# Performance work log

Measured on AMD Instinct MI355X. Metric: run time of the kernel, lower is better.

Reference implementation:

```python
import jax, jax.numpy as jnp
import numpy as np

N_NODES = 50000


def _add_self_loops(edge_index, num_nodes):
    loop = jnp.arange(num_nodes, dtype=edge_index.dtype)
    src = jnp.concatenate([edge_index[0], loop])
    dst = jnp.concatenate([edge_index[1], loop])
    return src, dst


def _gcn_norm(src, dst, num_nodes, dtype):
    # symmetric normalization: deg^{-1/2}[src] * deg^{-1/2}[dst]
    deg = jax.ops.segment_sum(jnp.ones_like(dst, dtype=dtype), dst,
                              num_segments=num_nodes)
    dinv = jnp.where(deg > 0, jax.lax.rsqrt(deg), 0.0).astype(dtype)
    return dinv[src] * dinv[dst]


def _gcn_conv(x, src, dst, norm, W, b, num_nodes):
    h = x @ W                                  # [N, out]
    msg = norm[:, None] * h[src]               # [E', out] gather
    agg = jax.ops.segment_sum(msg, dst, num_segments=num_nodes)  # scatter-add
    return agg + b


def setup_inputs() -> dict:
    key = jax.random.key(0)
    k1, k2, k3, k4 = jax.random.split(key, 4)
    x = jax.random.normal(k1, (N_NODES, 64), dtype=jnp.float32)
    edge_index = jax.random.randint(k2, (2, 800000), 0, N_NODES, dtype=jnp.int64)
    W1 = jax.random.normal(k3, (64, 64), dtype=jnp.float32) * (1.0 / np.sqrt(64))
    b1 = jnp.zeros((64,), dtype=jnp.float32)
    W2 = jax.random.normal(k4, (64, 37), dtype=jnp.float32) * (1.0 / np.sqrt(64))
    b2 = jnp.zeros((37,), dtype=jnp.float32)
    return {"x": x, "edge_index": edge_index, "W1": W1, "b1": b1,
            "W2": W2, "b2": b2}


def reference(x, edge_index, W1, b1, W2, b2):
    n = x.shape[0]
    src, dst = _add_self_loops(edge_index, n)
    norm = _gcn_norm(src, dst, n, x.dtype)
    h = _gcn_conv(x, src, dst, norm, W1, b1, n)
    h = jax.nn.relu(h)
    out = _gcn_conv(h, src, dst, norm, W2, b2, n)
    return out
```

## Files before the change

### kernel.cpp

```cpp
#include <hip/hip_runtime.h>
#include <hip/hip_fp16.h>

#define F_OUT 37
#define BSHIFT 7
#define BSIZE 128
#define CAP 3072
#define STAGE_CAP 3072
#define XS_STRIDE 68

__device__ __forceinline__ short4 pack4(float a, float b, float c, float d) {
    union { __half2 h2[2]; short4 s; } u;
    u.h2[0] = __floats2half2_rn(a, b);
    u.h2[1] = __floats2half2_rn(c, d);
    return u.s;
}
__device__ __forceinline__ float4 unpack4(short4 v) {
    union { short4 s; __half2 h2[2]; } u;
    u.s = v;
    float2 lo = __half22float2(u.h2[0]);
    float2 hi = __half22float2(u.h2[1]);
    return make_float4(lo.x, lo.y, hi.x, hi.y);
}


__global__ void init_gcur(int* __restrict__ gcur, int nb) {
    int t = blockIdx.x * blockDim.x + threadIdx.x;
    if (t < nb) gcur[t * 16] = t * CAP;
}

__global__ __launch_bounds__(256) void bucketA(const int* __restrict__ src,
                                               const int* __restrict__ dst,
                                               int E, int C, int nb,
                                               int* __restrict__ gcur,
                                               unsigned* __restrict__ bedge) {
    __shared__ unsigned stage[STAGE_CAP];
    __shared__ int lcnt[400];
    __shared__ int lbase[400];
    int t = threadIdx.x;
    int e0 = blockIdx.x * C;
    int cnt = E - e0; if (cnt > C) cnt = C; if (cnt <= 0) return;

    for (int i = t; i < nb; i += 256) lcnt[i] = 0;
    __syncthreads();
    for (int i = t; i < cnt; i += 256) {
        int s = src[e0 + i], d = dst[e0 + i];
        int b = d >> BSHIFT;
        atomicAdd(&lcnt[b], 1);
        stage[i] = ((unsigned)b << 23) | ((unsigned)(d & (BSIZE - 1)) << 16) | (unsigned)s;
    }
    __syncthreads();
    for (int i = t; i < nb; i += 256)
        lbase[i] = lcnt[i] ? atomicAdd(&gcur[i * 16], lcnt[i]) : 0;
    __syncthreads();
    for (int i = t; i < nb; i += 256) lcnt[i] = 0;
    __syncthreads();
    for (int i = t; i < cnt; i += 256) {
        unsigned w = stage[i];
        int b = w >> 23;
        int pos = lbase[b] + atomicAdd(&lcnt[b], 1);
        bedge[pos] = w & 0x7FFFFFu;
    }
}

__global__ __launch_bounds__(512) void scan_buckets(const int* __restrict__ gcur,
                                                    int nb, int E, int n,
                                                    int* __restrict__ bstart,
                                                    int* __restrict__ rowptr) {
    __shared__ int s[512];
    int t = threadIdx.x;
    int v = (t < nb) ? (gcur[t * 16] - t * CAP) : 0;
    s[t] = v;
    __syncthreads();
    for (int o = 1; o < 512; o <<= 1) {
        int a = (t >= o) ? s[t - o] : 0;
        __syncthreads();
        s[t] += a;
        __syncthreads();
    }
    if (t < nb) bstart[t] = s[t] - v;
    if (t == 0) rowptr[n] = E;
}

__global__ __launch_bounds__(256) void bucketB(const unsigned* __restrict__ bedge,
                                               const int* __restrict__ gcur,
                                               const int* __restrict__ bstart,
                                               int n,
                                               int* __restrict__ rowptr,
                                               int* __restrict__ srcIdx,
                                               float* __restrict__ dinv) {
    __shared__ int hcnt[BSIZE], hoff[BSIZE], hcur[BSIZE], tmp[BSIZE];
    int b = blockIdx.x;
    int t = threadIdx.x;
    int cntb = gcur[b * 16] - b * CAP;
    int base = bstart[b];
    const unsigned* ed = bedge + (size_t)b * CAP;

    if (t < BSIZE) { hcnt[t] = 0; hcur[t] = 0; }
    __syncthreads();
    for (int i = t; i < cntb; i += 256) atomicAdd(&hcnt[ed[i] >> 16], 1);
    __syncthreads();
    if (t < BSIZE) tmp[t] = hcnt[t];
    __syncthreads();
    for (int o = 1; o < BSIZE; o <<= 1) {
        int a = (t < BSIZE && t >= o) ? tmp[t - o] : 0;
        __syncthreads();
        if (t < BSIZE) tmp[t] += a;
        __syncthreads();
    }
    if (t < BSIZE) hoff[t] = tmp[t] - hcnt[t];
    __syncthreads();
    int node = b * BSIZE + t;
    if (t < BSIZE && node < n) {
        rowptr[node] = base + hoff[t];
        dinv[node] = rsqrtf(1.0f + (float)hcnt[t]);
    }
    for (int i = t; i < cntb; i += 256) {
        unsigned w = ed[i];
        int dloc = w >> 16;
        int pos = base + hoff[dloc] + atomicAdd(&hcur[dloc], 1);
        srcIdx[pos] = (int)(w & 0xFFFFu);
    }
}


#define MICRO_STEP(XI, ACC)                                                    \
    do {                                                                       \
        ACC[0] += XI.x * w0.x; ACC[1] += XI.x * w0.y;                          \
        ACC[2] += XI.x * w0.z; ACC[3] += XI.x * w0.w;                          \
        ACC[0] += XI.y * w1.x; ACC[1] += XI.y * w1.y;                          \
        ACC[2] += XI.y * w1.z; ACC[3] += XI.y * w1.w;                          \
        ACC[0] += XI.z * w2.x; ACC[1] += XI.z * w2.y;                          \
        ACC[2] += XI.z * w2.z; ACC[3] += XI.z * w2.w;                          \
        ACC[0] += XI.w * w3.x; ACC[1] += XI.w * w3.y;                          \
        ACC[2] += XI.w * w3.z; ACC[3] += XI.w * w3.w;                          \
    } while (0)

__global__ __launch_bounds__(256, 4) void gemm64(const float* __restrict__ x,
                                                 const float* __restrict__ W,
                                                 const float* __restrict__ dinv,
                                                 short4* __restrict__ hsv, int n) {
    __shared__ float Xs[64 * XS_STRIDE];
    __shared__ float Ws[64 * 64];
    int t = threadIdx.x;
    const float4* W4 = (const float4*)W;
#pragma unroll
    for (int i = 0; i < 4; ++i)
        ((float4*)Ws)[t + i * 256] = W4[t + i * 256];
    int row0 = blockIdx.x * 64;
#pragma unroll
    for (int i = 0; i < 4; ++i) {
        int idx = i * 256 + t;
        int r = idx >> 4, k4 = idx & 15;
        int grow = row0 + r;
        float4 v = (grow < n) ? ((const float4*)x)[(size_t)grow * 16 + k4]
                              : make_float4(0.f, 0.f, 0.f, 0.f);
        *(float4*)&Xs[r * XS_STRIDE + k4 * 4] = v;
    }
    __syncthreads();

    int tc = t & 15, tr = t >> 4;
    float a0[4] = {0.f, 0.f, 0.f, 0.f};
    float a1[4] = {0.f, 0.f, 0.f, 0.f};
    float a2[4] = {0.f, 0.f, 0.f, 0.f};
    float a3[4] = {0.f, 0.f, 0.f, 0.f};

#pragma unroll 2
    for (int k = 0; k < 64; k += 4) {
        float4 w0 = *(const float4*)&Ws[(k + 0) * 64 + 4 * tc];
        float4 w1 = *(const float4*)&Ws[(k + 1) * 64 + 4 * tc];
        float4 w2 = *(const float4*)&Ws[(k + 2) * 64 + 4 * tc];
        float4 w3 = *(const float4*)&Ws[(k + 3) * 64 + 4 * tc];
        float4 x0 = *(const float4*)&Xs[(4 * tr + 0) * XS_STRIDE + k];
        float4 x1 = *(const float4*)&Xs[(4 * tr + 1) * XS_STRIDE + k];
        float4 x2 = *(const float4*)&Xs[(4 * tr + 2) * XS_STRIDE + k];
        float4 x3 = *(const float4*)&Xs[(4 * tr + 3) * XS_STRIDE + k];
        MICRO_STEP(x0, a0);
        MICRO_STEP(x1, a1);
        MICRO_STEP(x2, a2);
        MICRO_STEP(x3, a3);
    }

#define STORE64(ACC, R)                                                        \
    do {                                                                       \
        int row = row0 + 4 * tr + (R);                                         \
        if (row < n) {                                                         \
            float dd = dinv[row];                                              \
            hsv[(size_t)row * 16 + tc] =                                       \
                pack4(ACC[0] * dd, ACC[1] * dd, ACC[2] * dd, ACC[3] * dd);     \
        }                                                                      \
    } while (0)
    STORE64(a0, 0); STORE64(a1, 1); STORE64(a2, 2); STORE64(a3, 3);
#undef STORE64
}

__global__ __launch_bounds__(256, 4) void gemm37(const short4* __restrict__ h1v,
                                                 const float* __restrict__ W,
                                                 short4* __restrict__ g40v, int n) {
    __shared__ float Xs[64 * XS_STRIDE];
    __shared__ float Ws[64 * 64];
    int t = threadIdx.x;
    for (int i = t; i < 64 * 64; i += 256) {
        int k = i >> 6, c = i & 63;
        Ws[i] = (c < F_OUT) ? W[k * F_OUT + c] : 0.f;
    }
    int row0 = blockIdx.x * 64;
#pragma unroll
    for (int i = 0; i < 4; ++i) {
        int idx = i * 256 + t;
        int r = idx >> 4, k4 = idx & 15;
        int grow = row0 + r;
        float4 v = (grow < n) ? unpack4(h1v[(size_t)grow * 16 + k4])
                              : make_float4(0.f, 0.f, 0.f, 0.f);
        *(float4*)&Xs[r * XS_STRIDE + k4 * 4] = v;
    }
    __syncthreads();

    int tc = t & 15, tr = t >> 4;
    float a0[4] = {0.f, 0.f, 0.f, 0.f};
    float a1[4] = {0.f, 0.f, 0.f, 0.f};
    float a2[4] = {0.f, 0.f, 0.f, 0.f};
    float a3[4] = {0.f, 0.f, 0.f, 0.f};

#pragma unroll 2
    for (int k = 0; k < 64; k += 4) {
        float4 w0 = *(const float4*)&Ws[(k + 0) * 64 + 4 * tc];
        float4 w1 = *(const float4*)&Ws[(k + 1) * 64 + 4 * tc];
        float4 w2 = *(const float4*)&Ws[(k + 2) * 64 + 4 * tc];
        float4 w3 = *(const float4*)&Ws[(k + 3) * 64 + 4 * tc];
        float4 x0 = *(const float4*)&Xs[(4 * tr + 0) * XS_STRIDE + k];
        float4 x1 = *(const float4*)&Xs[(4 * tr + 1) * XS_STRIDE + k];
        float4 x2 = *(const float4*)&Xs[(4 * tr + 2) * XS_STRIDE + k];
        float4 x3 = *(const float4*)&Xs[(4 * tr + 3) * XS_STRIDE + k];
        MICRO_STEP(x0, a0);
        MICRO_STEP(x1, a1);
        MICRO_STEP(x2, a2);
        MICRO_STEP(x3, a3);
    }

    if (tc < 10) {
        int row = row0 + 4 * tr;
        if (row < n)
            g40v[(size_t)row * 10 + tc] = pack4(a0[0], a0[1], a0[2], a0[3]);
        if (row + 1 < n)
            g40v[(size_t)(row + 1) * 10 + tc] = pack4(a1[0], a1[1], a1[2], a1[3]);
        if (row + 2 < n)
            g40v[(size_t)(row + 2) * 10 + tc] = pack4(a2[0], a2[1], a2[2], a2[3]);
        if (row + 3 < n)
            g40v[(size_t)(row + 3) * 10 + tc] = pack4(a3[0], a3[1], a3[2], a3[3]);
    }
}


#define ACCP4(A, B, C, D)                                                      \
    acc.x += (A.x + B.x) + (C.x + D.x);                                        \
    acc.y += (A.y + B.y) + (C.y + D.y);                                        \
    acc.z += (A.z + B.z) + (C.z + D.z);                                        \
    acc.w += (A.w + B.w) + (C.w + D.w);

__global__ void agg64_kernel(const int* __restrict__ rowptr,
                             const int* __restrict__ srcIdx,
                             const float* __restrict__ dinv,
                             const short4* __restrict__ hsv,
                             const float* __restrict__ bias,
                             short4* __restrict__ outv, int n) {
    int t = blockIdx.x * blockDim.x + threadIdx.x;
    int d = t >> 4, sub = t & 15;
    if (d >= n) return;
    int gbase = threadIdx.x & 48;
    float4 acc = unpack4(hsv[(size_t)d * 16 + sub]);
    int beg = rowptr[d], end = rowptr[d + 1];
    int j = beg;
#define LD64(Q) float4 v##Q = unpack4(hsv[(size_t)__shfl(myIdx, gbase + Q) * 16 + sub]);
    for (; j + 16 <= end; j += 16) {
        int myIdx = srcIdx[j + sub];
        LD64(0) LD64(1) LD64(2) LD64(3) LD64(4) LD64(5) LD64(6) LD64(7)
        LD64(8) LD64(9) LD64(10) LD64(11) LD64(12) LD64(13) LD64(14) LD64(15)
        ACCP4(v0, v1, v2, v3) ACCP4(v4, v5, v6, v7)
        ACCP4(v8, v9, v10, v11) ACCP4(v12, v13, v14, v15)
    }
    if (j + 8 <= end) {
        int myIdx = srcIdx[j + sub];
        LD64(0) LD64(1) LD64(2) LD64(3) LD64(4) LD64(5) LD64(6) LD64(7)
        ACCP4(v0, v1, v2, v3) ACCP4(v4, v5, v6, v7)
        j += 8;
    }
    if (j + 4 <= end) {
        int s0 = srcIdx[j], s1 = srcIdx[j + 1], s2 = srcIdx[j + 2], s3 = srcIdx[j + 3];
        float4 v0 = unpack4(hsv[(size_t)s0 * 16 + sub]);
        float4 v1 = unpack4(hsv[(size_t)s1 * 16 + sub]);
        float4 v2 = unpack4(hsv[(size_t)s2 * 16 + sub]);
        float4 v3 = unpack4(hsv[(size_t)s3 * 16 + sub]);
        ACCP4(v0, v1, v2, v3)
        j += 4;
    }
    for (; j < end; ++j) {
        float4 v = unpack4(hsv[(size_t)srcIdx[j] * 16 + sub]);
        acc.x += v.x; acc.y += v.y; acc.z += v.z; acc.w += v.w;
    }
#undef LD64
    float dd = dinv[d];
    float4 b = ((const float4*)bias)[sub];
    outv[(size_t)d * 16 + sub] =
        pack4(fmaxf(acc.x * dd + b.x, 0.f) * dd,
              fmaxf(acc.y * dd + b.y, 0.f) * dd,
              fmaxf(acc.z * dd + b.z, 0.f) * dd,
              fmaxf(acc.w * dd + b.w, 0.f) * dd);
}

__global__ void agg40_kernel(const int* __restrict__ rowptr,
                             const int* __restrict__ srcIdx,
                             const float* __restrict__ dinv,
                             const short4* __restrict__ g4v,
                             const float* __restrict__ bias,
                             float* __restrict__ out, int n) {
    int t = blockIdx.x * blockDim.x + threadIdx.x;
    int d = t >> 4, sub = t & 15;
    if (d >= n) return;
    int gbase = threadIdx.x & 48;
    bool act = sub < 10;
    float4 acc = make_float4(0.f, 0.f, 0.f, 0.f);
    if (act) acc = unpack4(g4v[(size_t)d * 10 + sub]);
    int beg = rowptr[d], end = rowptr[d + 1];
    int j = beg;
#define SH40(Q) int s##Q = __shfl(myIdx, gbase + Q);
#define G40(Q)  float4 v##Q = unpack4(g4v[(size_t)s##Q * 10 + sub]);
    for (; j + 16 <= end; j += 16) {
        int myIdx = srcIdx[j + sub];
        SH40(0) SH40(1) SH40(2) SH40(3) SH40(4) SH40(5) SH40(6) SH40(7)
        SH40(8) SH40(9) SH40(10) SH40(11) SH40(12) SH40(13) SH40(14) SH40(15)
        if (act) {
            G40(0) G40(1) G40(2) G40(3) G40(4) G40(5) G40(6) G40(7)
            G40(8) G40(9) G40(10) G40(11) G40(12) G40(13) G40(14) G40(15)
            ACCP4(v0, v1, v2, v3) ACCP4(v4, v5, v6, v7)
            ACCP4(v8, v9, v10, v11) ACCP4(v12, v13, v14, v15)
        }
    }
    if (j + 8 <= end) {
        int myIdx = srcIdx[j + sub];
        SH40(0) SH40(1) SH40(2) SH40(3) SH40(4) SH40(5) SH40(6) SH40(7)
        if (act) {
            G40(0) G40(1) G40(2) G40(3) G40(4) G40(5) G40(6) G40(7)
            ACCP4(v0, v1, v2, v3) ACCP4(v4, v5, v6, v7)
        }
        j += 8;
    }
    if (j + 4 <= end) {
        int s0 = srcIdx[j], s1 = srcIdx[j + 1], s2 = srcIdx[j + 2], s3 = srcIdx[j + 3];
        if (act) {
            float4 v0 = unpack4(g4v[(size_t)s0 * 10 + sub]);
            float4 v1 = unpack4(g4v[(size_t)s1 * 10 + sub]);
            float4 v2 = unpack4(g4v[(size_t)s2 * 10 + sub]);
            float4 v3 = unpack4(g4v[(size_t)s3 * 10 + sub]);
            ACCP4(v0, v1, v2, v3)
        }
        j += 4;
    }
    for (; j < end; ++j) {
        int s = srcIdx[j];
        if (act) {
            float4 v = unpack4(g4v[(size_t)s * 10 + sub]);
            acc.x += v.x; acc.y += v.y; acc.z += v.z; acc.w += v.w;
        }
    }
#undef SH40
#undef G40
    if (act) {
        float dd = dinv[d];
        int c0 = 4 * sub;
        float* o = &out[(size_t)d * F_OUT + c0];
        o[0] = acc.x * dd + bias[c0];
        if (c0 + 1 < F_OUT) o[1] = acc.y * dd + bias[c0 + 1];
        if (c0 + 2 < F_OUT) o[2] = acc.z * dd + bias[c0 + 2];
        if (c0 + 3 < F_OUT) o[3] = acc.w * dd + bias[c0 + 3];
    }
}

extern "C" void kernel_launch(void* const* d_in, const int* in_sizes, int n_in,
                              void* d_out, int out_size, void* d_ws, size_t ws_size,
                              hipStream_t stream) {
    const float* x  = (const float*)d_in[0];
    const int*   ei = (const int*)d_in[1];
    const float* W1 = (const float*)d_in[2];
    const float* b1 = (const float*)d_in[3];
    const float* W2 = (const float*)d_in[4];
    const float* b2 = (const float*)d_in[5];
    float* out = (float*)d_out;

    const int n = in_sizes[0] / 64;
    const int E = in_sizes[1] / 2;
    const int* src = ei;
    const int* dst = ei + E;

    const int nb = (n + BSIZE - 1) >> BSHIFT;
    const int nblkA = (E + STAGE_CAP - 1) / STAGE_CAP;
    const int C = (E + nblkA - 1) / nblkA;

    char* p = (char*)d_ws;
    int*   gcur   = (int*)p;   p += (size_t)nb * 16 * 4;
    int*   bstart = (int*)p;   p += (size_t)((nb + 3) & ~3) * 4;
    int*   rowptr = (int*)p;   p += (size_t)(n + 4) * 4;
    float* dinv   = (float*)p; p += (size_t)n * 4;
    int*   srcIdx = (int*)p;   p += (size_t)(E + 16) * 4;
    short4* hsv   = (short4*)p; p += (size_t)n * 64 * 2;
    short4* h1v   = (short4*)p; p += (size_t)n * 64 * 2;
    unsigned* bedge = (unsigned*)hsv;
    short4* g40v  = hsv;

    init_gcur<<<(nb + 255) / 256, 256, 0, stream>>>(gcur, nb);
    bucketA<<<nblkA, 256, 0, stream>>>(src, dst, E, C, nb, gcur, bedge);
    scan_buckets<<<1, 512, 0, stream>>>(gcur, nb, E, n, bstart, rowptr);
    bucketB<<<nb, 256, 0, stream>>>(bedge, gcur, bstart, n, rowptr, srcIdx, dinv);

    const int gemmBlocks = (n + 63) / 64;
    const int aggBlocks  = (n * 16 + 255) / 256;

    gemm64<<<gemmBlocks, 256, 0, stream>>>(x, W1, dinv, hsv, n);
    agg64_kernel<<<aggBlocks, 256, 0, stream>>>(rowptr, srcIdx, dinv, hsv, b1, h1v, n);

    gemm37<<<gemmBlocks, 256, 0, stream>>>(h1v, W2, g40v, n);
    agg40_kernel<<<aggBlocks, 256, 0, stream>>>(rowptr, srcIdx, dinv, g40v, b2, out, n);
}
```

Measured before the change: 114.9 us.

## Split layer-1 feature table into two column slices for cache-friendly aggregation

Splits the 64-wide half-precision hidden features into two 32-column tables, each 3.2MB, and runs the first aggregation as two block halves that each gather from one slice. With the working set of each half smaller, random neighbour gathers are more likely to hit in L2/MALL instead of going to HBM. The cost is reading the CSR indices twice and launching twice as many 8-lane groups per node. It also doubles the edge-bucketing stage capacity, which halves the number of bucketA blocks.

Result: no change. 113.3 us (-1.4%).

```diff
diff --git a/kernel.cpp b/kernel.cpp
--- a/kernel.cpp
+++ b/kernel.cpp
@@ -5,7 +5,7 @@
 #define BSHIFT 7
 #define BSIZE 128
 #define CAP 3072
-#define STAGE_CAP 3072
+#define STAGE_CAP 6144
 #define XS_STRIDE 68
 
 __device__ __forceinline__ short4 pack4(float a, float b, float c, float d) {
@@ -138,7 +138,8 @@
 __global__ __launch_bounds__(256, 4) void gemm64(const float* __restrict__ x,
                                                  const float* __restrict__ W,
                                                  const float* __restrict__ dinv,
-                                                 short4* __restrict__ hsv, int n) {
+                                                 short4* __restrict__ hv0,
+                                                 short4* __restrict__ hv1, int n) {
     __shared__ float Xs[64 * XS_STRIDE];
     __shared__ float Ws[64 * 64];
     int t = threadIdx.x;
@@ -180,12 +181,14 @@
         MICRO_STEP(x3, a3);
     }
 
+    short4* tab = (tc < 8) ? hv0 : hv1;
+    int lc = tc & 7;
 #define STORE64(ACC, R)                                                        \
     do {                                                                       \
         int row = row0 + 4 * tr + (R);                                         \
         if (row < n) {                                                         \
             float dd = dinv[row];                                              \
-            hsv[(size_t)row * 16 + tc] =                                       \
+            tab[(size_t)row * 8 + lc] =                                        \
                 pack4(ACC[0] * dd, ACC[1] * dd, ACC[2] * dd, ACC[3] * dd);     \
         }                                                                      \
     } while (0)
@@ -193,7 +196,8 @@
 #undef STORE64
 }
 
-__global__ __launch_bounds__(256, 4) void gemm37(const short4* __restrict__ h1v,
+__global__ __launch_bounds__(256, 4) void gemm37(const short4* __restrict__ h1v0,
+                                                 const short4* __restrict__ h1v1,
                                                  const float* __restrict__ W,
                                                  short4* __restrict__ g40v, int n) {
     __shared__ float Xs[64 * XS_STRIDE];
@@ -209,8 +213,10 @@
         int idx = i * 256 + t;
         int r = idx >> 4, k4 = idx & 15;
         int grow = row0 + r;
-        float4 v = (grow < n) ? unpack4(h1v[(size_t)grow * 16 + k4])
-                              : make_float4(0.f, 0.f, 0.f, 0.f);
+        float4 v = make_float4(0.f, 0.f, 0.f, 0.f);
+        if (grow < n)
+            v = unpack4((k4 < 8) ? h1v0[(size_t)grow * 8 + k4]
+                                 : h1v1[(size_t)grow * 8 + (k4 - 8)]);
         *(float4*)&Xs[r * XS_STRIDE + k4 * 4] = v;
     }
     __syncthreads();
@@ -257,50 +263,60 @@
     acc.z += (A.z + B.z) + (C.z + D.z);                                        \
     acc.w += (A.w + B.w) + (C.w + D.w);
 
-__global__ void agg64_kernel(const int* __restrict__ rowptr,
-                             const int* __restrict__ srcIdx,
-                             const float* __restrict__ dinv,
-                             const short4* __restrict__ hsv,
-                             const float* __restrict__ bias,
-                             short4* __restrict__ outv, int n) {
-    int t = blockIdx.x * blockDim.x + threadIdx.x;
-    int d = t >> 4, sub = t & 15;
+__global__ void agg64s(const int* __restrict__ rowptr,
+                       const int* __restrict__ srcIdx,
+                       const float* __restrict__ dinv,
+                       const short4* __restrict__ t0,
+                       const short4* __restrict__ t1,
+                       const float* __restrict__ bias,
+                       short4* __restrict__ o0, short4* __restrict__ o1,
+                       int n, int halfBlocks) {
+    int slice = (blockIdx.x >= halfBlocks) ? 1 : 0;
+    int bx = blockIdx.x - slice * halfBlocks;
+    int t = bx * blockDim.x + threadIdx.x;
+    int d = t >> 3, sub = t & 7;
     if (d >= n) return;
-    int gbase = threadIdx.x & 48;
-    float4 acc = unpack4(hsv[(size_t)d * 16 + sub]);
+    const short4* tab = slice ? t1 : t0;
+    short4* outv = slice ? o1 : o0;
+    int gbase = threadIdx.x & 56;
+
+    float4 acc = unpack4(tab[(size_t)d * 8 + sub]);
     int beg = rowptr[d], end = rowptr[d + 1];
     int j = beg;
-#define LD64(Q) float4 v##Q = unpack4(hsv[(size_t)__shfl(myIdx, gbase + Q) * 16 + sub]);
+#define LDA8(Q) float4 va##Q = unpack4(tab[(size_t)__shfl(idxA, gbase + Q) * 8 + sub]);
+#define LDB8(Q) float4 vb##Q = unpack4(tab[(size_t)__shfl(idxB, gbase + Q) * 8 + sub]);
     for (; j + 16 <= end; j += 16) {
-        int myIdx = srcIdx[j + sub];
-        LD64(0) LD64(1) LD64(2) LD64(3) LD64(4) LD64(5) LD64(6) LD64(7)
-        LD64(8) LD64(9) LD64(10) LD64(11) LD64(12) LD64(13) LD64(14) LD64(15)
-        ACCP4(v0, v1, v2, v3) ACCP4(v4, v5, v6, v7)
-        ACCP4(v8, v9, v10, v11) ACCP4(v12, v13, v14, v15)
+        int idxA = srcIdx[j + sub];
+        int idxB = srcIdx[j + 8 + sub];
+        LDA8(0) LDA8(1) LDA8(2) LDA8(3) LDA8(4) LDA8(5) LDA8(6) LDA8(7)
+        LDB8(0) LDB8(1) LDB8(2) LDB8(3) LDB8(4) LDB8(5) LDB8(6) LDB8(7)
+        ACCP4(va0, va1, va2, va3) ACCP4(va4, va5, va6, va7)
+        ACCP4(vb0, vb1, vb2, vb3) ACCP4(vb4, vb5, vb6, vb7)
     }
     if (j + 8 <= end) {
-        int myIdx = srcIdx[j + sub];
-        LD64(0) LD64(1) LD64(2) LD64(3) LD64(4) LD64(5) LD64(6) LD64(7)
-        ACCP4(v0, v1, v2, v3) ACCP4(v4, v5, v6, v7)
+        int idxA = srcIdx[j + sub];
+        LDA8(0) LDA8(1) LDA8(2) LDA8(3) LDA8(4) LDA8(5) LDA8(6) LDA8(7)
+        ACCP4(va0, va1, va2, va3) ACCP4(va4, va5, va6, va7)
         j += 8;
     }
     if (j + 4 <= end) {
         int s0 = srcIdx[j], s1 = srcIdx[j + 1], s2 = srcIdx[j + 2], s3 = srcIdx[j + 3];
-        float4 v0 = unpack4(hsv[(size_t)s0 * 16 + sub]);
-        float4 v1 = unpack4(hsv[(size_t)s1 * 16 + sub]);
-        float4 v2 = unpack4(hsv[(size_t)s2 * 16 + sub]);
-        float4 v3 = unpack4(hsv[(size_t)s3 * 16 + sub]);
+        float4 v0 = unpack4(tab[(size_t)s0 * 8 + sub]);
+        float4 v1 = unpack4(tab[(size_t)s1 * 8 + sub]);
+        float4 v2 = unpack4(tab[(size_t)s2 * 8 + sub]);
+        float4 v3 = unpack4(tab[(size_t)s3 * 8 + sub]);
         ACCP4(v0, v1, v2, v3)
         j += 4;
     }
     for (; j < end; ++j) {
-        float4 v = unpack4(hsv[(size_t)srcIdx[j] * 16 + sub]);
+        float4 v = unpack4(tab[(size_t)srcIdx[j] * 8 + sub]);
         acc.x += v.x; acc.y += v.y; acc.z += v.z; acc.w += v.w;
     }
-#undef LD64
+#undef LDA8
+#undef LDB8
     float dd = dinv[d];
-    float4 b = ((const float4*)bias)[sub];
-    outv[(size_t)d * 16 + sub] =
+    float4 b = ((const float4*)bias)[slice * 8 + sub];
+    outv[(size_t)d * 8 + sub] =
         pack4(fmaxf(acc.x * dd + b.x, 0.f) * dd,
               fmaxf(acc.y * dd + b.y, 0.f) * dd,
               fmaxf(acc.z * dd + b.z, 0.f) * dd,
@@ -401,10 +417,12 @@
     int*   rowptr = (int*)p;   p += (size_t)(n + 4) * 4;
     float* dinv   = (float*)p; p += (size_t)n * 4;
     int*   srcIdx = (int*)p;   p += (size_t)(E + 16) * 4;
-    short4* hsv   = (short4*)p; p += (size_t)n * 64 * 2;
-    short4* h1v   = (short4*)p; p += (size_t)n * 64 * 2;
-    unsigned* bedge = (unsigned*)hsv;
-    short4* g40v  = hsv;
+    short4* hv0   = (short4*)p; p += (size_t)n * 32 * 2;
+    short4* hv1   = (short4*)p; p += (size_t)n * 32 * 2;
+    short4* h1v0  = (short4*)p; p += (size_t)n * 32 * 2;
+    short4* h1v1  = (short4*)p; p += (size_t)n * 32 * 2;
+    unsigned* bedge = (unsigned*)hv0;
+    short4* g40v  = hv0;
 
     init_gcur<<<(nb + 255) / 256, 256, 0, stream>>>(gcur, nb);
     bucketA<<<nblkA, 256, 0, stream>>>(src, dst, E, C, nb, gcur, bedge);
@@ -412,11 +430,13 @@
     bucketB<<<nb, 256, 0, stream>>>(bedge, gcur, bstart, n, rowptr, srcIdx, dinv);
 
     const int gemmBlocks = (n + 63) / 64;
-    const int aggBlocks  = (n * 16 + 255) / 256;
-
-    gemm64<<<gemmBlocks, 256, 0, stream>>>(x, W1, dinv, hsv, n);
-    agg64_kernel<<<aggBlocks, 256, 0, stream>>>(rowptr, srcIdx, dinv, hsv, b1, h1v, n);
-
-    gemm37<<<gemmBlocks, 256, 0, stream>>>(h1v, W2, g40v, n);
-    agg40_kernel<<<aggBlocks, 256, 0, stream>>>(rowptr, srcIdx, dinv, g40v, b2, out, n);
-}
+    const int half8 = (n * 8 + 255) / 256;
+    const int aggBlocks16 = (n * 16 + 255) / 256;
+
+    gemm64<<<gemmBlocks, 256, 0, stream>>>(x, W1, dinv, hv0, hv1, n);
+    agg64s<<<2 * half8, 256, 0, stream>>>(rowptr, srcIdx, dinv, hv0, hv1, b1,
+                                          h1v0, h1v1, n, half8);
+
+    gemm37<<<gemmBlocks, 256, 0, stream>>>(h1v0, h1v1, W2, g40v, n);
+    agg40_kernel<<<aggBlocks16, 256, 0, stream>>>(rowptr, srcIdx, dinv, g40v, b2, out, n);
+}
```

## Drop bucket scan kernel, use padded CSR with begin/end arrays and split g40 table

Applied to the files above, without the earlier changes.

Removes the init_gcur and scan_buckets kernels: bucket counters are zeroed with a memset and each bucket's edges stay at a fixed CAP-padded offset, so rows are addressed through separate rowbeg/rowend arrays instead of a compact rowptr. The 37-wide second-layer features are stored as a 64-byte table plus an 8-byte side table, so each gather in agg40 touches aligned lines rather than 80-byte rows. STAGE_CAP is doubled, which halves the number of bucketA blocks and uses more shared memory per block. The padded srcIdx needs more workspace, and any bucket holding more than CAP edges would overflow.

Result: faster. 110.8 us, median of 2 (-3.6%).

```diff
diff --git a/kernel.cpp b/kernel.cpp
--- a/kernel.cpp
+++ b/kernel.cpp
@@ -5,7 +5,7 @@
 #define BSHIFT 7
 #define BSIZE 128
 #define CAP 3072
-#define STAGE_CAP 3072
+#define STAGE_CAP 6144
 #define XS_STRIDE 68
 
 __device__ __forceinline__ short4 pack4(float a, float b, float c, float d) {
@@ -22,11 +22,6 @@
     return make_float4(lo.x, lo.y, hi.x, hi.y);
 }
 
-
-__global__ void init_gcur(int* __restrict__ gcur, int nb) {
-    int t = blockIdx.x * blockDim.x + threadIdx.x;
-    if (t < nb) gcur[t * 16] = t * CAP;
-}
 
 __global__ __launch_bounds__(256) void bucketA(const int* __restrict__ src,
                                                const int* __restrict__ dst,
@@ -57,43 +52,24 @@
     for (int i = t; i < cnt; i += 256) {
         unsigned w = stage[i];
         int b = w >> 23;
-        int pos = lbase[b] + atomicAdd(&lcnt[b], 1);
+        int pos = b * CAP + lbase[b] + atomicAdd(&lcnt[b], 1);
         bedge[pos] = w & 0x7FFFFFu;
     }
-}
-
-__global__ __launch_bounds__(512) void scan_buckets(const int* __restrict__ gcur,
-                                                    int nb, int E, int n,
-                                                    int* __restrict__ bstart,
-                                                    int* __restrict__ rowptr) {
-    __shared__ int s[512];
-    int t = threadIdx.x;
-    int v = (t < nb) ? (gcur[t * 16] - t * CAP) : 0;
-    s[t] = v;
-    __syncthreads();
-    for (int o = 1; o < 512; o <<= 1) {
-        int a = (t >= o) ? s[t - o] : 0;
-        __syncthreads();
-        s[t] += a;
-        __syncthreads();
-    }
-    if (t < nb) bstart[t] = s[t] - v;
-    if (t == 0) rowptr[n] = E;
 }
 
 __global__ __launch_bounds__(256) void bucketB(const unsigned* __restrict__ bedge,
                                                const int* __restrict__ gcur,
-                                               const int* __restrict__ bstart,
                                                int n,
-                                               int* __restrict__ rowptr,
+                                               int* __restrict__ rowbeg,
+                                               int* __restrict__ rowend,
                                                int* __restrict__ srcIdx,
                                                float* __restrict__ dinv) {
     __shared__ int hcnt[BSIZE], hoff[BSIZE], hcur[BSIZE], tmp[BSIZE];
     int b = blockIdx.x;
     int t = threadIdx.x;
-    int cntb = gcur[b * 16] - b * CAP;
-    int base = bstart[b];
-    const unsigned* ed = bedge + (size_t)b * CAP;
+    int cntb = gcur[b * 16];
+    int base = b * CAP;
+    const unsigned* ed = bedge + (size_t)base;
 
     if (t < BSIZE) { hcnt[t] = 0; hcur[t] = 0; }
     __syncthreads();
@@ -111,7 +87,8 @@
     __syncthreads();
     int node = b * BSIZE + t;
     if (t < BSIZE && node < n) {
-        rowptr[node] = base + hoff[t];
+        rowbeg[node] = base + hoff[t];
+        rowend[node] = base + hoff[t] + hcnt[t];
         dinv[node] = rsqrtf(1.0f + (float)hcnt[t]);
     }
     for (int i = t; i < cntb; i += 256) {
@@ -195,7 +172,8 @@
 
 __global__ __launch_bounds__(256, 4) void gemm37(const short4* __restrict__ h1v,
                                                  const float* __restrict__ W,
-                                                 short4* __restrict__ g40v, int n) {
+                                                 short4* __restrict__ g32v,
+                                                 short4* __restrict__ g8v, int n) {
     __shared__ float Xs[64 * XS_STRIDE];
     __shared__ float Ws[64 * 64];
     int t = threadIdx.x;
@@ -238,15 +216,17 @@
     }
 
     if (tc < 10) {
-        int row = row0 + 4 * tr;
-        if (row < n)
-            g40v[(size_t)row * 10 + tc] = pack4(a0[0], a0[1], a0[2], a0[3]);
-        if (row + 1 < n)
-            g40v[(size_t)(row + 1) * 10 + tc] = pack4(a1[0], a1[1], a1[2], a1[3]);
-        if (row + 2 < n)
-            g40v[(size_t)(row + 2) * 10 + tc] = pack4(a2[0], a2[1], a2[2], a2[3]);
-        if (row + 3 < n)
-            g40v[(size_t)(row + 3) * 10 + tc] = pack4(a3[0], a3[1], a3[2], a3[3]);
+#define STORE37(ACC, R)                                                        \
+        do {                                                                   \
+            int row = row0 + 4 * tr + (R);                                     \
+            if (row < n) {                                                     \
+                short4 pv = pack4(ACC[0], ACC[1], ACC[2], ACC[3]);             \
+                if (tc < 8) g32v[(size_t)row * 8 + tc] = pv;                   \
+                else        g8v[(size_t)row * 2 + (tc - 8)] = pv;              \
+            }                                                                  \
+        } while (0)
+        STORE37(a0, 0); STORE37(a1, 1); STORE37(a2, 2); STORE37(a3, 3);
+#undef STORE37
     }
 }
 
@@ -257,7 +237,8 @@
     acc.z += (A.z + B.z) + (C.z + D.z);                                        \
     acc.w += (A.w + B.w) + (C.w + D.w);
 
-__global__ void agg64_kernel(const int* __restrict__ rowptr,
+__global__ void agg64_kernel(const int* __restrict__ rowbeg,
+                             const int* __restrict__ rowend,
                              const int* __restrict__ srcIdx,
                              const float* __restrict__ dinv,
                              const short4* __restrict__ hsv,
@@ -268,7 +249,7 @@
     if (d >= n) return;
     int gbase = threadIdx.x & 48;
     float4 acc = unpack4(hsv[(size_t)d * 16 + sub]);
-    int beg = rowptr[d], end = rowptr[d + 1];
+    int beg = rowbeg[d], end = rowend[d];
     int j = beg;
 #define LD64(Q) float4 v##Q = unpack4(hsv[(size_t)__shfl(myIdx, gbase + Q) * 16 + sub]);
     for (; j + 16 <= end; j += 16) {
@@ -307,10 +288,12 @@
               fmaxf(acc.w * dd + b.w, 0.f) * dd);
 }
 
-__global__ void agg40_kernel(const int* __restrict__ rowptr,
+__global__ void agg40_kernel(const int* __restrict__ rowbeg,
+                             const int* __restrict__ rowend,
                              const int* __restrict__ srcIdx,
                              const float* __restrict__ dinv,
-                             const short4* __restrict__ g4v,
+                             const short4* __restrict__ g32v,
+                             const short4* __restrict__ g8v,
                              const float* __restrict__ bias,
                              float* __restrict__ out, int n) {
     int t = blockIdx.x * blockDim.x + threadIdx.x;
@@ -318,12 +301,14 @@
     if (d >= n) return;
     int gbase = threadIdx.x & 48;
     bool act = sub < 10;
+    const short4* tab = (sub < 8) ? (g32v + sub) : (g8v + (sub - 8));
+    size_t stride = (sub < 8) ? 8 : 2;
     float4 acc = make_float4(0.f, 0.f, 0.f, 0.f);
-    if (act) acc = unpack4(g4v[(size_t)d * 10 + sub]);
-    int beg = rowptr[d], end = rowptr[d + 1];
+    if (act) acc = unpack4(tab[(size_t)d * stride]);
+    int beg = rowbeg[d], end = rowend[d];
     int j = beg;
 #define SH40(Q) int s##Q = __shfl(myIdx, gbase + Q);
-#define G40(Q)  float4 v##Q = unpack4(g4v[(size_t)s##Q * 10 + sub]);
+#define G40(Q)  float4 v##Q = unpack4(tab[(size_t)s##Q * stride]);
     for (; j + 16 <= end; j += 16) {
         int myIdx = srcIdx[j + sub];
         SH40(0) SH40(1) SH40(2) SH40(3) SH40(4) SH40(5) SH40(6) SH40(7)
@@ -347,10 +332,10 @@
     if (j + 4 <= end) {
         int s0 = srcIdx[j], s1 = srcIdx[j + 1], s2 = srcIdx[j + 2], s3 = srcIdx[j + 3];
         if (act) {
-            float4 v0 = unpack4(g4v[(size_t)s0 * 10 + sub]);
-            float4 v1 = unpack4(g4v[(size_t)s1 * 10 + sub]);
-            float4 v2 = unpack4(g4v[(size_t)s2 * 10 + sub]);
-            float4 v3 = unpack4(g4v[(size_t)s3 * 10 + sub]);
+            float4 v0 = unpack4(tab[(size_t)s0 * stride]);
+            float4 v1 = unpack4(tab[(size_t)s1 * stride]);
+            float4 v2 = unpack4(tab[(size_t)s2 * stride]);
+            float4 v3 = unpack4(tab[(size_t)s3 * stride]);
             ACCP4(v0, v1, v2, v3)
         }
         j += 4;
@@ -358,7 +343,7 @@
     for (; j < end; ++j) {
         int s = srcIdx[j];
         if (act) {
-            float4 v = unpack4(g4v[(size_t)s * 10 + sub]);
+            float4 v = unpack4(tab[(size_t)s * stride]);
             acc.x += v.x; acc.y += v.y; acc.z += v.z; acc.w += v.w;
         }
     }
@@ -397,26 +382,26 @@
 
     char* p = (char*)d_ws;
     int*   gcur   = (int*)p;   p += (size_t)nb * 16 * 4;
-    int*   bstart = (int*)p;   p += (size_t)((nb + 3) & ~3) * 4;
-    int*   rowptr = (int*)p;   p += (size_t)(n + 4) * 4;
+    int*   rowbeg = (int*)p;   p += (size_t)(n + 4) * 4;
+    int*   rowend = (int*)p;   p += (size_t)(n + 4) * 4;
     float* dinv   = (float*)p; p += (size_t)n * 4;
-    int*   srcIdx = (int*)p;   p += (size_t)(E + 16) * 4;
+    int*   srcIdx = (int*)p;   p += ((size_t)nb * CAP + 16) * 4;
     short4* hsv   = (short4*)p; p += (size_t)n * 64 * 2;
     short4* h1v   = (short4*)p; p += (size_t)n * 64 * 2;
     unsigned* bedge = (unsigned*)hsv;
-    short4* g40v  = hsv;
-
-    init_gcur<<<(nb + 255) / 256, 256, 0, stream>>>(gcur, nb);
+    short4* g32v  = hsv;
+    short4* g8v   = hsv + (size_t)n * 8;
+
+    hipMemsetAsync(gcur, 0, (size_t)nb * 16 * 4, stream);
     bucketA<<<nblkA, 256, 0, stream>>>(src, dst, E, C, nb, gcur, bedge);
-    scan_buckets<<<1, 512, 0, stream>>>(gcur, nb, E, n, bstart, rowptr);
-    bucketB<<<nb, 256, 0, stream>>>(bedge, gcur, bstart, n, rowptr, srcIdx, dinv);
+    bucketB<<<nb, 256, 0, stream>>>(bedge, gcur, n, rowbeg, rowend, srcIdx, dinv);
 
     const int gemmBlocks = (n + 63) / 64;
     const int aggBlocks  = (n * 16 + 255) / 256;
 
     gemm64<<<gemmBlocks, 256, 0, stream>>>(x, W1, dinv, hsv, n);
-    agg64_kernel<<<aggBlocks, 256, 0, stream>>>(rowptr, srcIdx, dinv, hsv, b1, h1v, n);
-
-    gemm37<<<gemmBlocks, 256, 0, stream>>>(h1v, W2, g40v, n);
-    agg40_kernel<<<aggBlocks, 256, 0, stream>>>(rowptr, srcIdx, dinv, g40v, b2, out, n);
-}
+    agg64_kernel<<<aggBlocks, 256, 0, stream>>>(rowbeg, rowend, srcIdx, dinv, hsv, b1, h1v, n);
+
+    gemm37<<<gemmBlocks, 256, 0, stream>>>(h1v, W2, g32v, g8v, n);
+    agg40_kernel<<<aggBlocks, 256, 0, stream>>>(rowbeg, rowend, srcIdx, dinv, g32v, g8v, b2, out, n);
+}
```
